# Optimization experiments

Measured on AMD Instinct MI355X. Metric: run time of the kernel, lower is better.

Reference implementation:

```python
import jax, jax.numpy as jnp
import numpy as np

# ---- module constants (from init_kwargs) ----
EMBED_DIM = 384
NUM_HYPEREDGES = 128
TOPK = 64
SPATIAL_SHAPE = (16, 32, 32)  # D, H, W -> N = 16384
SPACING = (2.0, 1.0, 1.0)
SPATIAL_WEIGHT = 0.1
B, N, C = 4, 16 * 32 * 32, EMBED_DIM


def _l2norm(x, axis=-1, eps=1e-12):
    n = jnp.linalg.norm(x, axis=axis, keepdims=True)
    return x / jnp.maximum(n, eps)


def _get_3d_coords():
    D, H, W = SPATIAL_SHAPE
    z = jnp.arange(D, dtype=jnp.float32) * SPACING[0]
    y = jnp.arange(H, dtype=jnp.float32) * SPACING[1]
    x = jnp.arange(W, dtype=jnp.float32) * SPACING[2]
    zz, yy, xx = jnp.meshgrid(z, y, x, indexing='ij')
    return jnp.stack([zz, yy, xx], axis=-1).reshape(-1, 3)  # (N, 3)


def setup_inputs() -> dict:
    key = jax.random.key(0)
    k1, k2 = jax.random.split(key)
    node_features = jax.random.normal(k1, (B, N, C), dtype=jnp.float32)
    class_token = jax.random.normal(k2, (1, 1, C), dtype=jnp.float32)
    temperature = jnp.ones((1,), dtype=jnp.float32) * 0.07
    return {"node_features": node_features, "class_token": class_token, "temperature": temperature}


def reference(node_features, class_token, temperature):
    Ne = NUM_HYPEREDGES
    w = SPATIAL_WEIGHT
    temp = temperature[0]

    nodes_n = _l2norm(node_features)                      # (B, N, C)

    # Step 1: center sampling by semantic similarity to class token
    ct_n = _l2norm(jnp.broadcast_to(class_token, (B, 1, C)))
    scores = jnp.einsum('boc,bnc->bn', ct_n, nodes_n) / temp  # (B, N)
    _, center_idx = jax.lax.top_k(scores, Ne)             # (B, Ne)

    # Gather centers and compute cosine sim of every center vs all nodes
    centers = jnp.take_along_axis(node_features, center_idx[:, :, None], axis=1)  # (B, Ne, C)
    centers_n = _l2norm(centers)
    sem_sim = jnp.einsum('bec,bnc->ben', centers_n, nodes_n) / temp  # (B, Ne, N)

    # Spatial bias (normalized distance from each center voxel)
    coords = _get_3d_coords()                             # (N, 3)
    center_coords = coords[center_idx]                    # (B, Ne, 3)
    diff = coords[None, None, :, :] - center_coords[:, :, None, :]  # (B, Ne, N, 3)
    dist = jnp.linalg.norm(diff, axis=-1)                 # (B, Ne, N)
    dist = dist / (jnp.max(dist, axis=-1, keepdims=True) + 1e-8)
    combined = (1.0 - w) * sem_sim + w * (1.0 - dist)     # (B, Ne, N)

    # Per-hyperedge top-K neighbors -> incidence matrix H (B, N, Ne)
    _, nbr_idx = jax.lax.top_k(combined, TOPK)            # (B, Ne, K)
    b_ix = jnp.arange(B)[:, None, None]
    e_ix = jnp.arange(Ne)[None, :, None]
    Hmat = jnp.zeros((B, N, Ne), dtype=node_features.dtype)
    Hmat = Hmat.at[b_ix, nbr_idx, e_ix].set(1.0)
    return Hmat
```

## Files before the change

### kernel.cpp

```cpp
#include <hip/hip_runtime.h>
#include <math.h>

#define BB 4
#define NN 16384
#define CC 384
#define NE 128
#define KK 64
#define EQCAP 256
#define ROWP 130

typedef unsigned short ushort_t;
typedef __attribute__((ext_vector_type(8))) short bf16x8;
typedef __attribute__((ext_vector_type(4))) float f32x4;
#define MFMA(a, b, c) __builtin_amdgcn_mfma_f32_16x16x32_bf16(a, b, c, 0, 0, 0)

__device__ inline unsigned fkey(float f) {
    unsigned b = __float_as_uint(f);
    return (b & 0x80000000u) ? ~b : (b | 0x80000000u);
}
__device__ inline ushort_t bf16rne(float f) {
    unsigned u = __float_as_uint(f);
    unsigned r = u + 0x7FFFu + ((u >> 16) & 1u);
    return (ushort_t)(r >> 16);
}
__device__ inline float bf16tof(ushort_t h) {
    return __uint_as_float(((unsigned)h) << 16);
}
#define CVT2(fa, fb, outh, outl) { \
    ushort_t ha = bf16rne(fa), hb = bf16rne(fb); \
    float la = (fa) - bf16tof(ha), lb = (fb) - bf16tof(hb); \
    outh = (unsigned)ha | ((unsigned)hb << 16); \
    outl = (unsigned)bf16rne(la) | ((unsigned)bf16rne(lb) << 16); }

__device__ inline void bin_select(unsigned* hist, int t, int* wsum,
                                  int* sh_bin, int* sh_r, int r) {
    int lane = t & 63, wid = t >> 6;
    int c = (t < 256) ? (int)hist[t] : 0;
    int x = c;
#pragma unroll
    for (int off = 1; off < 64; off <<= 1) {
        int v = __shfl_down(x, off, 64);
        if (lane + off < 64) x += v;
    }
    if (lane == 0 && wid < 4) wsum[wid] = x;
    __syncthreads();
    if (t < 256) {
        int add = 0;
        for (int w2 = wid + 1; w2 < 4; ++w2) add += wsum[w2];
        int S_incl = x + add;
        int S_excl = S_incl - c;
        if (S_excl < r && S_incl >= r) { *sh_bin = t; *sh_r = r - S_excl; }
    }
    __syncthreads();
}

__global__ __launch_bounds__(256) void k_scores(const float* __restrict__ nf,
                                                const float* __restrict__ ct,
                                                unsigned* __restrict__ keys,
                                                float* __restrict__ invn) {
    int wave = threadIdx.x >> 6;
    int lane = threadIdx.x & 63;
    int row  = blockIdx.x * 4 + wave;
    const float* x = nf + (size_t)row * CC;
    float4 a  = ((const float4*)x)[lane];
    float2 c2 = ((const float2*)(x + 256))[lane];
    float4 ta = ((const float4*)ct)[lane];
    float2 tc = ((const float2*)(ct + 256))[lane];
    float ss = a.x*a.x + a.y*a.y + a.z*a.z + a.w*a.w + c2.x*c2.x + c2.y*c2.y;
    float dt = ta.x*a.x + ta.y*a.y + ta.z*a.z + ta.w*a.w + tc.x*c2.x + tc.y*c2.y;
#pragma unroll
    for (int off = 32; off; off >>= 1) {
        ss += __shfl_xor(ss, off, 64);
        dt += __shfl_xor(dt, off, 64);
    }
    if (lane == 0) {
        float inv = 1.0f / fmaxf(sqrtf(ss), 1e-12f);
        invn[row] = inv;
        keys[row] = fkey(dt * inv);
    }
}

__global__ __launch_bounds__(1024) void k_top128(const unsigned* __restrict__ keys,
                                                 int* __restrict__ cidx) {
    __shared__ unsigned hist[256];
    __shared__ int wsum[4];
    __shared__ int sh_bin, sh_r;
    __shared__ unsigned cu[NE];
    __shared__ int cil[NE];
    __shared__ int eqi[EQCAP];
    __shared__ int cnt_gt, cnt_eq;
    int b = blockIdx.x;
    int t = threadIdx.x;
    const uint4* rowv = (const uint4*)(keys + b * NN);
    if (t == 0) { cnt_gt = 0; cnt_eq = 0; }
    unsigned prefix = 0;
    int r = NE;
#pragma unroll
    for (int pass = 0; pass < 4; ++pass) {
        int shift = 24 - 8 * pass;
        unsigned hm = (pass == 0) ? 0u : (0xFFFFFFFFu << (shift + 8));
        if (t < 256) hist[t] = 0;
        __syncthreads();
#pragma unroll
        for (int i = 0; i < 4; ++i) {
            uint4 u = rowv[t + 1024 * i];
            if ((u.x & hm) == (prefix & hm)) atomicAdd(&hist[(u.x >> shift) & 255], 1u);
            if ((u.y & hm) == (prefix & hm)) atomicAdd(&hist[(u.y >> shift) & 255], 1u);
            if ((u.z & hm) == (prefix & hm)) atomicAdd(&hist[(u.z >> shift) & 255], 1u);
            if ((u.w & hm) == (prefix & hm)) atomicAdd(&hist[(u.w >> shift) & 255], 1u);
        }
        __syncthreads();
        bin_select(hist, t, wsum, &sh_bin, &sh_r, r);
        prefix |= ((unsigned)sh_bin) << shift;
        r = sh_r;
        __syncthreads();
    }
    unsigned T = prefix;
#pragma unroll
    for (int i = 0; i < 4; ++i) {
        uint4 u = rowv[t + 1024 * i];
        int nb = 4 * (t + 1024 * i);
        unsigned vv[4] = {u.x, u.y, u.z, u.w};
#pragma unroll
        for (int cmp = 0; cmp < 4; ++cmp) {
            if (vv[cmp] > T) {
                int p = atomicAdd(&cnt_gt, 1);
                cu[p] = vv[cmp]; cil[p] = nb + cmp;
            } else if (vv[cmp] == T) {
                int p = atomicAdd(&cnt_eq, 1);
                if (p < EQCAP) eqi[p] = nb + cmp;
            }
        }
    }
    __syncthreads();
    int ne = cnt_eq < EQCAP ? cnt_eq : EQCAP;
    if (t < ne) {
        int mine = eqi[t], rk = 0;
        for (int j = 0; j < ne; ++j) rk += (eqi[j] < mine);
        if (rk < r) { int p = cnt_gt + rk; cu[p] = T; cil[p] = mine; }
    }
    __syncthreads();
    if (t < NE) {
        unsigned mu = cu[t]; int mi = cil[t], rk = 0;
#pragma unroll 4
        for (int j = 0; j < NE; ++j) {
            unsigned ou = cu[j]; int oi = cil[j];
            rk += (ou > mu) || (ou == mu && oi < mi);
        }
        cidx[b * NE + rk] = mi;
    }
}

__global__ __launch_bounds__(128) void k_centers(const float* __restrict__ nf,
                                                 const float* __restrict__ invn,
                                                 const int* __restrict__ cidx,
                                                 ushort_t* __restrict__ Ahi,
                                                 ushort_t* __restrict__ Alo,
                                                 float* __restrict__ meta) {
    int be = blockIdx.x;
    int b  = be >> 7;
    int ci = cidx[be];
    float inv = invn[b * NN + ci];
    const float* src = nf + ((size_t)b * NN + ci) * CC;
    for (int c = threadIdx.x; c < CC; c += 128) {
        float f = src[c] * inv;
        ushort_t h = bf16rne(f);
        Ahi[(size_t)be * CC + c] = h;
        Alo[(size_t)be * CC + c] = bf16rne(f - bf16tof(h));
    }
    if (threadIdx.x == 0) {
        float zc = (float)(ci >> 10) * 2.0f;
        float yc = (float)((ci >> 5) & 31);
        float xc = (float)(ci & 31);
        float mz = fmaxf(zc * zc, (30.f - zc) * (30.f - zc));
        float my = fmaxf(yc * yc, (31.f - yc) * (31.f - yc));
        float mx = fmaxf(xc * xc, (31.f - xc) * (31.f - xc));
        float md = sqrtf(mz + my + mx);
        meta[be * 4 + 0] = zc;
        meta[be * 4 + 1] = yc;
        meta[be * 4 + 2] = xc;
        meta[be * 4 + 3] = 1.0f / (md + 1e-8f);
    }
}

__global__ __launch_bounds__(256) void k_gemm(const float* __restrict__ nf,
                                              const ushort_t* __restrict__ Ahi,
                                              const ushort_t* __restrict__ Alo,
                                              const float* __restrict__ invn,
                                              const float* __restrict__ meta,
                                              const float* __restrict__ temp,
                                              unsigned* __restrict__ outk) {
    __shared__ ushort_t Ah[4][ROWP][8], Al_[4][ROWP][8], Bh[4][ROWP][8], Bl[4][ROWP][8];
    __shared__ float ms[NE * 4];
    __shared__ float invs_s[128];
    int b  = blockIdx.y;
    int n0 = blockIdx.x * 128;
    int t  = threadIdx.x;
    int w  = t >> 6, lane = t & 63;
    int quad = lane >> 4, mrow = lane & 15;
    int m0 = (w & 1) * 64, nw0 = (w >> 1) * 64;
    for (int i = t; i < NE * 4; i += 256) ms[i] = meta[b * NE * 4 + i];
    if (t < 128) invs_s[t] = invn[b * NN + n0 + t];
    f32x4 acc[4][4];
#pragma unroll
    for (int i = 0; i < 4; ++i)
#pragma unroll
        for (int j = 0; j < 4; ++j) acc[i][j] = (f32x4)0.f;
    const ushort_t* Abh = Ahi + (size_t)b * NE * CC;
    const ushort_t* Abl = Alo + (size_t)b * NE * CC;
    const float* Bb = nf + ((size_t)b * NN + n0) * CC;
    for (int kt = 0; kt < CC; kt += 32) {
        __syncthreads();
#pragma unroll
        for (int i = 0; i < 2; ++i) {
            int c = t + 256 * i;
            int e = c >> 2, k8 = c & 3;
            int off = e * CC + kt + k8 * 8;
            *(uint4*)&Ah[k8][e][0]  = *(const uint4*)(Abh + off);
            *(uint4*)&Al_[k8][e][0] = *(const uint4*)(Abl + off);
        }
#pragma unroll
        for (int i = 0; i < 2; ++i) {
            int c = t + 256 * i;
            int n = c >> 2, k8 = c & 3;
            const float* src = Bb + (size_t)n * CC + kt + k8 * 8;
            float4 fa = ((const float4*)src)[0];
            float4 fb = ((const float4*)src)[1];
            uint4 ph, pl;
            CVT2(fa.x, fa.y, ph.x, pl.x);
            CVT2(fa.z, fa.w, ph.y, pl.y);
            CVT2(fb.x, fb.y, ph.z, pl.z);
            CVT2(fb.z, fb.w, ph.w, pl.w);
            *(uint4*)&Bh[k8][n][0] = ph;
            *(uint4*)&Bl[k8][n][0] = pl;
        }
        __syncthreads();
        bf16x8 afh[4], afl[4], bfh[4], bfl[4];
#pragma unroll
        for (int i = 0; i < 4; ++i) {
            afh[i] = *(const bf16x8*)&Ah[quad][m0 + i * 16 + mrow][0];
            afl[i] = *(const bf16x8*)&Al_[quad][m0 + i * 16 + mrow][0];
            bfh[i] = *(const bf16x8*)&Bh[quad][nw0 + i * 16 + mrow][0];
            bfl[i] = *(const bf16x8*)&Bl[quad][nw0 + i * 16 + mrow][0];
        }
#pragma unroll
        for (int i = 0; i < 4; ++i)
#pragma unroll
            for (int j = 0; j < 4; ++j) {
                acc[i][j] = MFMA(afh[i], bfh[j], acc[i][j]);
                acc[i][j] = MFMA(afh[i], bfl[j], acc[i][j]);
                acc[i][j] = MFMA(afl[i], bfh[j], acc[i][j]);
            }
    }
    float scale = 0.9f / temp[0];
#pragma unroll
    for (int j = 0; j < 4; ++j) {
        int nloc = nw0 + j * 16 + (lane & 15);
        int n = n0 + nloc;
        float invnn = invs_s[nloc];
        float zf = (float)(n >> 10) * 2.0f;
        float yf = (float)((n >> 5) & 31);
        float xf = (float)(n & 31);
#pragma unroll
        for (int i = 0; i < 4; ++i) {
#pragma unroll
            for (int r = 0; r < 4; ++r) {
                int e = m0 + i * 16 + quad * 4 + r;
                float zc = ms[e * 4 + 0], yc = ms[e * 4 + 1], xc = ms[e * 4 + 2], ivd = ms[e * 4 + 3];
                float dz = zf - zc, dy = yf - yc, dx = xf - xc;
                float dist = sqrtf(dz * dz + dy * dy + dx * dx);
                float v = scale * invnn * acc[i][j][r] + 0.1f * (1.0f - dist * ivd);
                outk[((size_t)(b * NE + e)) * NN + n] = fkey(v);
            }
        }
    }
}

__global__ __launch_bounds__(1024) void k_top64(const unsigned* __restrict__ comb,
                                                int* __restrict__ sel) {
    __shared__ unsigned hist[256];
    __shared__ int wsum[4];
    __shared__ int sh_bin, sh_r;
    __shared__ int eqi[EQCAP];
    __shared__ int cnt_gt, cnt_eq;
    int be = blockIdx.x;
    int t  = threadIdx.x;
    const uint4* rowv = (const uint4*)(comb + (size_t)be * NN);
    if (t == 0) { cnt_gt = 0; cnt_eq = 0; }
    unsigned prefix = 0;
    int r = KK;
#pragma unroll
    for (int pass = 0; pass < 4; ++pass) {
        int shift = 24 - 8 * pass;
        unsigned hm = (pass == 0) ? 0u : (0xFFFFFFFFu << (shift + 8));
        if (t < 256) hist[t] = 0;
        __syncthreads();
#pragma unroll
        for (int i = 0; i < 4; ++i) {
            uint4 u = rowv[t + 1024 * i];
            if ((u.x & hm) == (prefix & hm)) atomicAdd(&hist[(u.x >> shift) & 255], 1u);
            if ((u.y & hm) == (prefix & hm)) atomicAdd(&hist[(u.y >> shift) & 255], 1u);
            if ((u.z & hm) == (prefix & hm)) atomicAdd(&hist[(u.z >> shift) & 255], 1u);
            if ((u.w & hm) == (prefix & hm)) atomicAdd(&hist[(u.w >> shift) & 255], 1u);
        }
        __syncthreads();
        bin_select(hist, t, wsum, &sh_bin, &sh_r, r);
        prefix |= ((unsigned)sh_bin) << shift;
        r = sh_r;
        __syncthreads();
    }
    unsigned T = prefix;
#pragma unroll
    for (int i = 0; i < 4; ++i) {
        uint4 u = rowv[t + 1024 * i];
        int nb = 4 * (t + 1024 * i);
        unsigned vv[4] = {u.x, u.y, u.z, u.w};
#pragma unroll
        for (int cmp = 0; cmp < 4; ++cmp) {
            if (vv[cmp] > T) {
                int p = atomicAdd(&cnt_gt, 1);
                sel[be * KK + p] = nb + cmp;
            } else if (vv[cmp] == T) {
                int p = atomicAdd(&cnt_eq, 1);
                if (p < EQCAP) eqi[p] = nb + cmp;
            }
        }
    }
    __syncthreads();
    int ne = cnt_eq < EQCAP ? cnt_eq : EQCAP;
    if (t < ne) {
        int mine = eqi[t], rk = 0;
        for (int j = 0; j < ne; ++j) rk += (eqi[j] < mine);
        if (rk < r) sel[be * KK + cnt_gt + rk] = mine;
    }
}

__global__ __launch_bounds__(256) void k_scatter(const int* __restrict__ sel,
                                                 float* __restrict__ H) {
    int gid = blockIdx.x * 256 + threadIdx.x;
    int b = gid >> 13;
    int e = (gid >> 6) & 127;
    int n = sel[gid];
    H[((size_t)b * NN + n) * NE + e] = 1.0f;
}

extern "C" void kernel_launch(void* const* d_in, const int* in_sizes, int n_in,
                              void* d_out, int out_size, void* d_ws, size_t ws_size,
                              hipStream_t stream) {
    const float* nf   = (const float*)d_in[0];
    const float* ct   = (const float*)d_in[1];
    const float* temp = (const float*)d_in[2];
    float* out = (float*)d_out;

    unsigned* keys = (unsigned*)d_ws;
    float* invn    = (float*)(keys + BB * NN);
    float* meta    = invn + BB * NN;
    ushort_t* Ahi  = (ushort_t*)(meta + BB * NE * 4);
    ushort_t* Alo  = Ahi + (size_t)BB * NE * CC;
    int* cidx      = (int*)(Alo + (size_t)BB * NE * CC);
    int* sel       = cidx + BB * NE;

    k_scores <<<BB * NN / 4, 256, 0, stream>>>(nf, ct, keys, invn);
    k_top128 <<<BB, 1024, 0, stream>>>(keys, cidx);
    k_centers<<<BB * NE, 128, 0, stream>>>(nf, invn, cidx, Ahi, Alo, meta);
    k_gemm   <<<dim3(NN / 128, BB), 256, 0, stream>>>(nf, Ahi, Alo, invn, meta, temp, (unsigned*)out);
    k_top64  <<<BB * NE, 1024, 0, stream>>>((const unsigned*)out, sel);
    hipMemsetAsync(d_out, 0, (size_t)BB * NN * NE * sizeof(float), stream);
    k_scatter<<<BB * NE * KK / 256, 256, 0, stream>>>(sel, out);
}
```

Measured before the change: 259.3 us.

## Fuse center gather into top-128, shrink GEMM N-tile, load A via LDS DMA

```diff
diff --git a/kernel.cpp b/kernel.cpp
--- a/kernel.cpp
+++ b/kernel.cpp
@@ -7,7 +7,6 @@
 #define NE 128
 #define KK 64
 #define EQCAP 256
-#define ROWP 130
 
 typedef unsigned short ushort_t;
 typedef __attribute__((ext_vector_type(8))) short bf16x8;
@@ -26,11 +25,22 @@
 __device__ inline float bf16tof(ushort_t h) {
     return __uint_as_float(((unsigned)h) << 16);
 }
-#define CVT2(fa, fb, outh, outl) { \
-    ushort_t ha = bf16rne(fa), hb = bf16rne(fb); \
-    float la = (fa) - bf16tof(ha), lb = (fb) - bf16tof(hb); \
-    outh = (unsigned)ha | ((unsigned)hb << 16); \
-    outl = (unsigned)bf16rne(la) | ((unsigned)bf16rne(lb) << 16); }
+__device__ inline void cvt2(float fa, float fb, unsigned& hp, unsigned& lp) {
+    unsigned ua = __float_as_uint(fa), ub = __float_as_uint(fb);
+    unsigned ra = ua + 0x8000u, rb = ub + 0x8000u;
+    hp = (ra >> 16) | (rb & 0xFFFF0000u);
+    float ha = __uint_as_float(ra & 0xFFFF0000u);
+    float hb = __uint_as_float(rb & 0xFFFF0000u);
+    float la = fa - ha, lb = fb - hb;
+    unsigned lra = __float_as_uint(la) + 0x8000u;
+    unsigned lrb = __float_as_uint(lb) + 0x8000u;
+    lp = (lra >> 16) | (lrb & 0xFFFF0000u);
+}
+__device__ inline void gload16(const void* g, void* l) {
+    __builtin_amdgcn_global_load_lds(
+        (const __attribute__((address_space(1))) void*)g,
+        (__attribute__((address_space(3))) void*)l, 16, 0, 0);
+}
 
 __device__ inline void bin_select(unsigned* hist, int t, int* wsum,
                                   int* sh_bin, int* sh_r, int r) {
@@ -81,7 +91,11 @@
 }
 
 __global__ __launch_bounds__(1024) void k_top128(const unsigned* __restrict__ keys,
-                                                 int* __restrict__ cidx) {
+                                                 const float* __restrict__ nf,
+                                                 const float* __restrict__ invn,
+                                                 ushort_t* __restrict__ Ahi,
+                                                 ushort_t* __restrict__ Alo,
+                                                 float* __restrict__ meta) {
     __shared__ unsigned hist[256];
     __shared__ int wsum[4];
     __shared__ int sh_bin, sh_r;
@@ -89,6 +103,7 @@
     __shared__ int cil[NE];
     __shared__ int eqi[EQCAP];
     __shared__ int cnt_gt, cnt_eq;
+    __shared__ int ocid[NE];
     int b = blockIdx.x;
     int t = threadIdx.x;
     const uint4* rowv = (const uint4*)(keys + b * NN);
@@ -147,28 +162,31 @@
             unsigned ou = cu[j]; int oi = cil[j];
             rk += (ou > mu) || (ou == mu && oi < mi);
         }
-        cidx[b * NE + rk] = mi;
-    }
-}
-
-__global__ __launch_bounds__(128) void k_centers(const float* __restrict__ nf,
-                                                 const float* __restrict__ invn,
-                                                 const int* __restrict__ cidx,
-                                                 ushort_t* __restrict__ Ahi,
-                                                 ushort_t* __restrict__ Alo,
-                                                 float* __restrict__ meta) {
-    int be = blockIdx.x;
-    int b  = be >> 7;
-    int ci = cidx[be];
-    float inv = invn[b * NN + ci];
-    const float* src = nf + ((size_t)b * NN + ci) * CC;
-    for (int c = threadIdx.x; c < CC; c += 128) {
-        float f = src[c] * inv;
-        ushort_t h = bf16rne(f);
-        Ahi[(size_t)be * CC + c] = h;
-        Alo[(size_t)be * CC + c] = bf16rne(f - bf16tof(h));
-    }
-    if (threadIdx.x == 0) {
+        ocid[rk] = mi;
+    }
+    __syncthreads();
+    {
+        int e = t >> 3, part = t & 7;
+        int ci = ocid[e];
+        float inv = invn[b * NN + ci];
+        const float4* src = (const float4*)(nf + ((size_t)b * NN + ci) * CC) + part * 12;
+        ushort_t* dh = Ahi + ((size_t)b * NE + e) * CC + part * 48;
+        ushort_t* dl = Alo + ((size_t)b * NE + e) * CC + part * 48;
+#pragma unroll
+        for (int i = 0; i < 12; ++i) {
+            float4 f = src[i];
+            f.x *= inv; f.y *= inv; f.z *= inv; f.w *= inv;
+            ushort4 h, l;
+            h.x = bf16rne(f.x); l.x = bf16rne(f.x - bf16tof(h.x));
+            h.y = bf16rne(f.y); l.y = bf16rne(f.y - bf16tof(h.y));
+            h.z = bf16rne(f.z); l.z = bf16rne(f.z - bf16tof(h.z));
+            h.w = bf16rne(f.w); l.w = bf16rne(f.w - bf16tof(h.w));
+            ((ushort4*)dh)[i] = h;
+            ((ushort4*)dl)[i] = l;
+        }
+    }
+    if (t < NE) {
+        int ci = ocid[t];
         float zc = (float)(ci >> 10) * 2.0f;
         float yc = (float)((ci >> 5) & 31);
         float xc = (float)(ci & 31);
@@ -176,6 +194,7 @@
         float my = fmaxf(yc * yc, (31.f - yc) * (31.f - yc));
         float mx = fmaxf(xc * xc, (31.f - xc) * (31.f - xc));
         float md = sqrtf(mz + my + mx);
+        int be = b * NE + t;
         meta[be * 4 + 0] = zc;
         meta[be * 4 + 1] = yc;
         meta[be * 4 + 2] = xc;
@@ -183,70 +202,77 @@
     }
 }
 
-__global__ __launch_bounds__(256) void k_gemm(const float* __restrict__ nf,
-                                              const ushort_t* __restrict__ Ahi,
-                                              const ushort_t* __restrict__ Alo,
-                                              const float* __restrict__ invn,
-                                              const float* __restrict__ meta,
-                                              const float* __restrict__ temp,
-                                              unsigned* __restrict__ outk) {
-    __shared__ ushort_t Ah[4][ROWP][8], Al_[4][ROWP][8], Bh[4][ROWP][8], Bl[4][ROWP][8];
+__global__ __launch_bounds__(256, 4) void k_gemm(const float* __restrict__ nf,
+                                                 const ushort_t* __restrict__ Ahi,
+                                                 const ushort_t* __restrict__ Alo,
+                                                 const float* __restrict__ invn,
+                                                 const float* __restrict__ meta,
+                                                 const float* __restrict__ temp,
+                                                 unsigned* __restrict__ outk) {
+    __shared__ ushort_t Ah[4096], Al[4096];
+    __shared__ ushort_t Bhs[2048], Bls[2048];
     __shared__ float ms[NE * 4];
-    __shared__ float invs_s[128];
+    __shared__ float invs_s[64];
     int b  = blockIdx.y;
-    int n0 = blockIdx.x * 128;
+    int n0 = blockIdx.x * 64;
     int t  = threadIdx.x;
-    int w  = t >> 6, lane = t & 63;
-    int quad = lane >> 4, mrow = lane & 15;
-    int m0 = (w & 1) * 64, nw0 = (w >> 1) * 64;
+    int w = t >> 6, lane = t & 63, quad = lane >> 4, mrow = lane & 15;
+    int m0 = (w & 1) * 64, nw0 = (w >> 1) * 32;
     for (int i = t; i < NE * 4; i += 256) ms[i] = meta[b * NE * 4 + i];
-    if (t < 128) invs_s[t] = invn[b * NN + n0 + t];
-    f32x4 acc[4][4];
+    if (t < 64) invs_s[t] = invn[b * NN + n0 + t];
+    f32x4 acc[4][2];
 #pragma unroll
     for (int i = 0; i < 4; ++i)
 #pragma unroll
-        for (int j = 0; j < 4; ++j) acc[i][j] = (f32x4)0.f;
+        for (int j = 0; j < 2; ++j) acc[i][j] = (f32x4)0.f;
     const ushort_t* Abh = Ahi + (size_t)b * NE * CC;
     const ushort_t* Abl = Alo + (size_t)b * NE * CC;
     const float* Bb = nf + ((size_t)b * NN + n0) * CC;
+    int bn = t >> 2, bk8 = t & 3;
+    const float* bsrc = Bb + (size_t)bn * CC + bk8 * 8;
+    ushort_t* bh_dst = &Bhs[(bk8 * 64 + bn) * 8];
+    ushort_t* bl_dst = &Bls[(bk8 * 64 + bn) * 8];
+    const ushort_t* agh0 = Abh + (size_t)(w * 16 + mrow) * CC + quad * 8;
+    const ushort_t* agh1 = Abh + (size_t)((w + 4) * 16 + mrow) * CC + quad * 8;
+    const ushort_t* agl0 = Abl + (size_t)(w * 16 + mrow) * CC + quad * 8;
+    const ushort_t* agl1 = Abl + (size_t)((w + 4) * 16 + mrow) * CC + quad * 8;
     for (int kt = 0; kt < CC; kt += 32) {
         __syncthreads();
-#pragma unroll
-        for (int i = 0; i < 2; ++i) {
-            int c = t + 256 * i;
-            int e = c >> 2, k8 = c & 3;
-            int off = e * CC + kt + k8 * 8;
-            *(uint4*)&Ah[k8][e][0]  = *(const uint4*)(Abh + off);
-            *(uint4*)&Al_[k8][e][0] = *(const uint4*)(Abl + off);
-        }
-#pragma unroll
-        for (int i = 0; i < 2; ++i) {
-            int c = t + 256 * i;
-            int n = c >> 2, k8 = c & 3;
-            const float* src = Bb + (size_t)n * CC + kt + k8 * 8;
-            float4 fa = ((const float4*)src)[0];
-            float4 fb = ((const float4*)src)[1];
+        gload16(agh0 + kt, &Ah[w * 512]);
+        gload16(agh1 + kt, &Ah[(w + 4) * 512]);
+        gload16(agl0 + kt, &Al[w * 512]);
+        gload16(agl1 + kt, &Al[(w + 4) * 512]);
+        {
+            const float4* bs = (const float4*)(bsrc + kt);
+            float4 f0 = bs[0];
+            float4 f1 = bs[1];
             uint4 ph, pl;
-            CVT2(fa.x, fa.y, ph.x, pl.x);
-            CVT2(fa.z, fa.w, ph.y, pl.y);
-            CVT2(fb.x, fb.y, ph.z, pl.z);
-            CVT2(fb.z, fb.w, ph.w, pl.w);
-            *(uint4*)&Bh[k8][n][0] = ph;
-            *(uint4*)&Bl[k8][n][0] = pl;
-        }
-        __syncthreads();
-        bf16x8 afh[4], afl[4], bfh[4], bfl[4];
+            cvt2(f0.x, f0.y, ph.x, pl.x);
+            cvt2(f0.z, f0.w, ph.y, pl.y);
+            cvt2(f1.x, f1.y, ph.z, pl.z);
+            cvt2(f1.z, f1.w, ph.w, pl.w);
+            *(uint4*)bh_dst = ph;
+            *(uint4*)bl_dst = pl;
+        }
+        __syncthreads();
+        bf16x8 afh[4], afl[4], bfh[2], bfl[2];
 #pragma unroll
         for (int i = 0; i < 4; ++i) {
-            afh[i] = *(const bf16x8*)&Ah[quad][m0 + i * 16 + mrow][0];
-            afl[i] = *(const bf16x8*)&Al_[quad][m0 + i * 16 + mrow][0];
-            bfh[i] = *(const bf16x8*)&Bh[quad][nw0 + i * 16 + mrow][0];
-            bfl[i] = *(const bf16x8*)&Bl[quad][nw0 + i * 16 + mrow][0];
+            int m = m0 + i * 16 + mrow;
+            int off = (m >> 4) * 512 + quad * 128 + (m & 15) * 8;
+            afh[i] = *(const bf16x8*)&Ah[off];
+            afl[i] = *(const bf16x8*)&Al[off];
+        }
+#pragma unroll
+        for (int j = 0; j < 2; ++j) {
+            int n = nw0 + j * 16 + mrow;
+            bfh[j] = *(const bf16x8*)&Bhs[(quad * 64 + n) * 8];
+            bfl[j] = *(const bf16x8*)&Bls[(quad * 64 + n) * 8];
         }
 #pragma unroll
         for (int i = 0; i < 4; ++i)
 #pragma unroll
-            for (int j = 0; j < 4; ++j) {
+            for (int j = 0; j < 2; ++j) {
                 acc[i][j] = MFMA(afh[i], bfh[j], acc[i][j]);
                 acc[i][j] = MFMA(afh[i], bfl[j], acc[i][j]);
                 acc[i][j] = MFMA(afl[i], bfh[j], acc[i][j]);
@@ -254,8 +280,8 @@
     }
     float scale = 0.9f / temp[0];
 #pragma unroll
-    for (int j = 0; j < 4; ++j) {
-        int nloc = nw0 + j * 16 + (lane & 15);
+    for (int j = 0; j < 2; ++j) {
+        int nloc = nw0 + j * 16 + mrow;
         int n = n0 + nloc;
         float invnn = invs_s[nloc];
         float zf = (float)(n >> 10) * 2.0f;
@@ -357,13 +383,11 @@
     float* meta    = invn + BB * NN;
     ushort_t* Ahi  = (ushort_t*)(meta + BB * NE * 4);
     ushort_t* Alo  = Ahi + (size_t)BB * NE * CC;
-    int* cidx      = (int*)(Alo + (size_t)BB * NE * CC);
-    int* sel       = cidx + BB * NE;
+    int* sel       = (int*)(Alo + (size_t)BB * NE * CC);
 
     k_scores <<<BB * NN / 4, 256, 0, stream>>>(nf, ct, keys, invn);
-    k_top128 <<<BB, 1024, 0, stream>>>(keys, cidx);
-    k_centers<<<BB * NE, 128, 0, stream>>>(nf, invn, cidx, Ahi, Alo, meta);
-    k_gemm   <<<dim3(NN / 128, BB), 256, 0, stream>>>(nf, Ahi, Alo, invn, meta, temp, (unsigned*)out);
+    k_top128 <<<BB, 1024, 0, stream>>>(keys, nf, invn, Ahi, Alo, meta);
+    k_gemm   <<<dim3(NN / 64, BB), 256, 0, stream>>>(nf, Ahi, Alo, invn, meta, temp, (unsigned*)out);
     k_top64  <<<BB * NE, 1024, 0, stream>>>((const unsigned*)out, sel);
     hipMemsetAsync(d_out, 0, (size_t)BB * NN * NE * sizeof(float), stream);
     k_scatter<<<BB * NE * KK / 256, 256, 0, stream>>>(sel, out);
```

Measured after the change: 287.2 us. 10.8% more time.
